# Optimization experiments

Measured on AMD Instinct MI355X. Metric: run time of the kernel, lower is better.

Reference implementation:

```python
import jax, jax.numpy as jnp
import numpy as np

B, NP1, D = 64, 1025, 256  # N+1 tokens, feature dim d (label dim makes d+1)
N_LAYER, N_HEAD = 4, 4
VAR = 0.02


def _pad_pq(allparam):
    """Build padded (d+1)x(d+1) P_full/Q_full for all layers/heads at once.
    P_full gets a 1 at [d, d]; Q_full is zero-padded."""
    L, H, _, d, _ = allparam.shape
    Pf = (jnp.zeros((L, H, d + 1, d + 1), allparam.dtype)
          .at[:, :, :d, :d].set(allparam[:, :, 0])
          .at[:, :, d, d].set(1.0))
    Qf = (jnp.zeros((L, H, d + 1, d + 1), allparam.dtype)
          .at[:, :, :d, :d].set(allparam[:, :, 1]))
    return Pf, Qf


def setup_inputs() -> dict:
    key = jax.random.key(0)
    k1, k2 = jax.random.split(key)
    Z = jax.random.normal(k1, (B, NP1, D + 1), dtype=jnp.float32)
    allparam = jax.random.normal(k2, (N_LAYER, N_HEAD, 2, D, D), dtype=jnp.float32) * VAR
    return {"Z": Z, "allparam": allparam}


def reference(Z, allparam):
    Bb, Np1, dp1 = Z.shape
    N = Np1 - 1
    Pf, Qf = _pad_pq(allparam)  # (L, H, d+1, d+1)
    # mask A = diag(1,...,1,0): equivalent to zeroing the last key token
    mask = jnp.ones((Np1,), Z.dtype).at[N].set(0.0)
    for l in range(allparam.shape[0]):
        # attn[b,h,n,m] = Z[b,n,:] @ Q_full[h] @ Z[b,m,:]
        attn = jnp.einsum('bni,hij,bmj->bhnm', Z, Qf[l], Z)
        attn = jax.nn.relu(attn)
        # key[b,h,m,i] = P_full[h] @ Z[b,m,:], last token masked out (A matrix)
        key_t = jnp.einsum('hij,bmj->bhmi', Pf[l], Z) * mask[None, None, :, None]
        # sum over heads fused into the einsum reduction; scale by 1/N
        res = jnp.einsum('bhnm,bhmi->bni', attn, key_t) / N
        Z = Z + res  # residual connection
    return Z
```

## Files before the change

### kernel.cpp

```cpp
#include <hip/hip_runtime.h>
#include <cstdint>
#include <cstddef>

#define B_    64
#define NP1   1025
#define N_    1024
#define D_    256
#define DP1   257
#define L_    4
#define H_    4
#define MT    1024
#define NCHE  32
#define IPAD  272
#define TR_   1024

typedef __bf16 bf16;
typedef bf16 bf16x4 __attribute__((ext_vector_type(4)));
typedef bf16 bf16x8 __attribute__((ext_vector_type(8)));
typedef float f32x4 __attribute__((ext_vector_type(4)));

__device__ __forceinline__ f32x4 mfma16(bf16x8 a, bf16x8 b, f32x4 c) {
    return __builtin_amdgcn_mfma_f32_16x16x32_bf16(a, b, c, 0, 0, 0);
}

__device__ __forceinline__ void async16(const void* g, void* l) {
    __builtin_amdgcn_global_load_lds(
        (const __attribute__((address_space(1))) void*)g,
        (__attribute__((address_space(3))) void*)l, 16, 0, 0);
}

__global__ void k_prep_pq(const float* __restrict__ ap,
                          bf16* __restrict__ Pb, bf16* __restrict__ Qt) {
    int idx = blockIdx.x * 256 + threadIdx.x;
    int j  = idx & 255;
    int i  = (idx >> 8) & 255;
    int lh = idx >> 16;
    const float* base = ap + (size_t)lh * 2 * D_ * D_;
    float p = base[i * D_ + j];
    float q = base[D_ * D_ + i * D_ + j];
    Pb[((size_t)lh * D_ + i) * D_ + j] = (bf16)p;
    Qt[((size_t)lh * D_ + j) * D_ + i] = (bf16)q;
}

__global__ __launch_bounds__(256) void k_zbt(const float* __restrict__ Z,
                                             bf16* __restrict__ Zb,
                                             bf16* __restrict__ ZbT) {
    __shared__ float t[64][65];
    int m0 = blockIdx.x * 64, j0 = blockIdx.y * 64, b = blockIdx.z;
    int c = threadIdx.x & 63, r0 = threadIdx.x >> 6;
#pragma unroll
    for (int s = 0; s < 16; s++) {
        int r = s * 4 + r0;
        int j = j0 + c;
        float v = (j < DP1) ? Z[((size_t)b * NP1 + m0 + r) * DP1 + j] : 0.f;
        t[r][c] = v;
        if (j < D_) Zb[((size_t)b * N_ + m0 + r) * D_ + j] = (bf16)v;
    }
    __syncthreads();
#pragma unroll
    for (int s = 0; s < 16; s++) {
        int rr = s * 4 + r0;
        int j = j0 + rr;
        if (j < DP1)
            ZbT[((size_t)b * DP1 + j) * MT + m0 + c] = (bf16)t[c][rr];
    }
}

__global__ __launch_bounds__(512, 1) void k_attn(const bf16* __restrict__ Zb,
                                                 const bf16* __restrict__ ZbT,
                                                 const bf16* __restrict__ Qt,
                                                 bf16* __restrict__ T,
                                                 bf16* __restrict__ Tlab,
                                                 int layer) {
    __shared__ bf16 zbS[2][32][256];
    __shared__ bf16 ztS[2][IPAD][32];
    __shared__ bf16 sl[8][32][40];

    const int tid  = threadIdx.x;
    const int id   = blockIdx.x;
    const int wave = tid >> 6, lane = tid & 63;
    const int quad = lane >> 4, l16 = lane & 15;

    const int xcd = id & 7, u = id >> 3;
    const int b   = xcd + 8 * (u & 7);
    const int bx  = u >> 3;
    const int n0w = bx * 256 + wave * 32;

    const bf16* Zbb  = Zb  + (size_t)b * N_ * D_;
    const bf16* ZbTb = ZbT + (size_t)b * DP1 * MT;

    const int zrow  = wave * 2 + (lane >> 5);
    const int zscol = ((lane & 31) ^ (zrow & 7)) * 8;
    const int krow  = wave * 16 + (lane >> 2);
    const int kscol = ((lane & 3) ^ ((lane >> 3) & 3)) * 8;
    const int xs    = l16 & 7;
    const int kf    = (l16 >> 1) & 3;

    auto stage = [&](int mc_, int p_) {
        int m0 = mc_ * 32;
        const bf16* zsrc = Zbb + (size_t)(m0 + zrow) * D_ + zscol;
#pragma unroll
        for (int t = 0; t < 2; t++)
            async16(zsrc + (size_t)t * 16 * D_, &zbS[p_][t * 16 + wave * 2][0]);
        const bf16* ksrc = ZbTb + (size_t)krow * MT + m0 + kscol;
#pragma unroll
        for (int t = 0; t < 2; t++)
            async16(ksrc + (size_t)t * 128 * MT, &ztS[p_][t * 128 + wave * 16][0]);
        if (wave == 0)
            async16(ksrc + (size_t)256 * MT, &ztS[p_][256][0]);
    };

    int p = 0;

    for (int h = 0; h < H_; h++) {
        const bf16* Qth = Qt + (size_t)(layer * H_ + h) * D_ * D_;

        if (h == 0) stage(0, 0);

        f32x4 acc[2][17];
#pragma unroll
        for (int ns = 0; ns < 2; ns++)
#pragma unroll
            for (int it = 0; it < 17; it++) acc[ns][it] = (f32x4){0.f, 0.f, 0.f, 0.f};

        bf16x8 zqa[2][8];
#pragma unroll 2
        for (int jc = 0; jc < 8; jc++) {
            f32x4 c00 = (f32x4){0.f,0.f,0.f,0.f}, c01 = c00, c10 = c00, c11 = c00;
#pragma unroll
            for (int kc = 0; kc < 8; kc++) {
                const bf16* qb = Qth + (size_t)(jc * 32 + l16) * D_ + kc * 32 + quad * 8;
                const bf16* az = Zbb + (size_t)(n0w + l16) * D_ + kc * 32 + quad * 8;
                bf16x8 q0 = *(const bf16x8*)(qb);
                bf16x8 q1 = *(const bf16x8*)(qb + 16 * D_);
                bf16x8 a0 = *(const bf16x8*)(az);
                bf16x8 a1 = *(const bf16x8*)(az + 16 * D_);
                c00 = mfma16(q0, a0, c00);
                c01 = mfma16(q0, a1, c01);
                c10 = mfma16(q1, a0, c10);
                c11 = mfma16(q1, a1, c11);
            }
            f32x4 cv[2][2] = {{c00, c01}, {c10, c11}};
#pragma unroll
            for (int jt = 0; jt < 2; jt++)
#pragma unroll
                for (int ns = 0; ns < 2; ns++) {
                    bf16x4 pk;
#pragma unroll
                    for (int r = 0; r < 4; r++) pk[r] = (bf16)cv[jt][ns][r];
                    *(bf16x4*)(&sl[wave][ns * 16 + l16][jt * 16 + quad * 4]) = pk;
                }
#pragma unroll
            for (int ns = 0; ns < 2; ns++)
                zqa[ns][jc] = *(const bf16x8*)(&sl[wave][ns * 16 + l16][quad * 8]);
        }

        if (h == 0) {
            asm volatile("s_waitcnt vmcnt(0)" ::: "memory");
            __builtin_amdgcn_s_barrier();
            __builtin_amdgcn_sched_barrier(0);
        }

        for (int cc = 0; cc < NCHE; cc++) {
            const bool haveNext = (cc + 1 < NCHE);
            if (haveNext) {
                int mcn = (h & 1) ? (NCHE - 2 - cc) : (cc + 1);
                stage(mcn, p ^ 1);
                if (wave == 0) asm volatile("s_waitcnt vmcnt(5)" ::: "memory");
                else           asm volatile("s_waitcnt vmcnt(4)" ::: "memory");
            } else {
                asm volatile("s_waitcnt vmcnt(0)" ::: "memory");
            }
            __builtin_amdgcn_s_barrier();
            __builtin_amdgcn_sched_barrier(0);

#pragma unroll
            for (int mt = 0; mt < 2; mt++) {
                f32x4 st0 = (f32x4){0.f,0.f,0.f,0.f}, st1 = st0;
                const bf16* zr = &zbS[p][mt * 16 + l16][0];
                __builtin_amdgcn_s_setprio(1);
#pragma unroll
                for (int kc = 0; kc < 8; kc++) {
                    bf16x8 az = *(const bf16x8*)(zr + (((kc * 4 + quad) ^ xs) * 8));
                    st0 = mfma16(az, zqa[0][kc], st0);
                    st1 = mfma16(az, zqa[1][kc], st1);
                }
                __builtin_amdgcn_s_setprio(0);
                bf16x4 p0, p1;
#pragma unroll
                for (int r = 0; r < 4; r++) {
                    p0[r] = (bf16)(st0[r] > 0.f ? st0[r] : 0.f);
                    p1[r] = (bf16)(st1[r] > 0.f ? st1[r] : 0.f);
                }
                *(bf16x4*)(&sl[wave][l16][mt * 16 + quad * 4])      = p0;
                *(bf16x4*)(&sl[wave][16 + l16][mt * 16 + quad * 4]) = p1;
            }
            bf16x8 sfrag[2];
#pragma unroll
            for (int ns = 0; ns < 2; ns++)
                sfrag[ns] = *(const bf16x8*)(&sl[wave][ns * 16 + l16][quad * 8]);

            __builtin_amdgcn_s_setprio(1);
#pragma unroll
            for (int it = 0; it < 17; it++) {
                const bf16* kr = &ztS[p][it * 16 + l16][0];
                bf16x8 bk = *(const bf16x8*)(kr + ((quad ^ kf) * 8));
                acc[0][it] = mfma16(sfrag[0], bk, acc[0][it]);
                acc[1][it] = mfma16(sfrag[1], bk, acc[1][it]);
            }
            __builtin_amdgcn_s_setprio(0);

            __builtin_amdgcn_sched_barrier(0);
            __builtin_amdgcn_s_barrier();
            if (haveNext) p ^= 1;
        }

        bf16* Th  = T    + (size_t)(b * H_ + h) * TR_ * D_;
        bf16* Tlh = Tlab + (size_t)(b * H_ + h) * TR_;
#pragma unroll
        for (int ns = 0; ns < 2; ns++)
#pragma unroll
            for (int it = 0; it < 17; it++)
#pragma unroll
                for (int r = 0; r < 4; r++) {
                    int n = n0w + ns * 16 + quad * 4 + r;
                    float v = acc[ns][it][r];
                    if (it < 16)
                        Th[(size_t)n * D_ + it * 16 + l16] = (bf16)v;
                    else if (l16 == 0)
                        Tlh[n] = (bf16)v;
                }
    }
}

__global__ __launch_bounds__(256, 2) void k_post(const bf16* __restrict__ T,
                                                 const bf16* __restrict__ Tlab,
                                                 const bf16* __restrict__ Pb,
                                                 const bf16* __restrict__ Zb,
                                                 const bf16* __restrict__ ZbT,
                                                 const bf16* __restrict__ Qt,
                                                 float* __restrict__ Z, int layer) {
    __shared__ float lz1[256];
    __shared__ float lzq[256];
    __shared__ float lsS[1024];
    __shared__ float lT[256];
    __shared__ float llab[256];

    const int tid  = threadIdx.x;
    const int id   = blockIdx.x;

    if (id >= 512) {
        const int b = id - 512;
        const bf16* Zbb  = Zb  + (size_t)b * N_ * D_;
        const bf16* tr   = ZbT + ((size_t)b * DP1 + tid) * MT;
        const bf16* zlab = ZbT + ((size_t)b * DP1 + D_) * MT;
        lz1[tid] = Z[((size_t)b * NP1 + N_) * DP1 + tid];
        float outacc = 0.f, labacc = 0.f;
        __syncthreads();
        for (int h = 0; h < H_; h++) {
            const bf16* Qth = Qt + (size_t)(layer * H_ + h) * D_ * D_;
            const bf16* Ph  = Pb + (size_t)(layer * H_ + h) * D_ * D_;
            {
                float a = 0.f;
                const bf16* qr = Qth + (size_t)tid * D_;
                for (int i8 = 0; i8 < 32; i8++) {
                    bf16x8 q = *(const bf16x8*)(qr + i8 * 8);
#pragma unroll
                    for (int k = 0; k < 8; k++) a += lz1[i8 * 8 + k] * (float)q[k];
                }
                lzq[tid] = a;
            }
            __syncthreads();
            for (int m = tid; m < N_; m += 256) {
                float a = 0.f;
                const bf16* zr = Zbb + (size_t)m * D_;
                for (int j8 = 0; j8 < 32; j8++) {
                    bf16x8 z8 = *(const bf16x8*)(zr + j8 * 8);
#pragma unroll
                    for (int k = 0; k < 8; k++) a += lzq[j8 * 8 + k] * (float)z8[k];
                }
                lsS[m] = a > 0.f ? a : 0.f;
            }
            __syncthreads();
            {
                float tv = 0.f;
                for (int m8 = 0; m8 < 128; m8++) {
                    bf16x8 t8 = *(const bf16x8*)(tr + m8 * 8);
#pragma unroll
                    for (int k = 0; k < 8; k++) tv += lsS[m8 * 8 + k] * (float)t8[k];
                }
                lT[tid] = tv;
            }
            for (int m = tid; m < N_; m += 256)
                labacc += lsS[m] * (float)zlab[m];
            __syncthreads();
            {
                const bf16* pr = Ph + (size_t)tid * D_;
                for (int j8 = 0; j8 < 32; j8++) {
                    bf16x8 p8 = *(const bf16x8*)(pr + j8 * 8);
#pragma unroll
                    for (int k = 0; k < 8; k++) outacc += lT[j8 * 8 + k] * (float)p8[k];
                }
            }
            __syncthreads();
        }
        const float inv = 1.0f / (float)N_;
        Z[((size_t)b * NP1 + N_) * DP1 + tid] += outacc * inv;
        llab[tid] = labacc;
        __syncthreads();
        if (tid == 0) {
            float s = 0.f;
            for (int t = 0; t < 256; t++) s += llab[t];
            Z[((size_t)b * NP1 + N_) * DP1 + D_] += s * inv;
        }
        return;
    }

    const int wave = tid >> 6, lane = tid & 63;
    const int quad = lane >> 4, l16 = lane & 15;
    const int xcd = id & 7, u = id >> 3;
    const int b   = xcd + 8 * (u & 3) + 32 * (u >> 5);
    const int bx  = (u >> 2) & 7;
    const int n0w = bx * 128 + wave * 32;

    f32x4 acc[2][16];
#pragma unroll
    for (int ns = 0; ns < 2; ns++)
#pragma unroll
        for (int it = 0; it < 16; it++) acc[ns][it] = (f32x4){0.f, 0.f, 0.f, 0.f};

    for (int h = 0; h < H_; h++) {
        const bf16* Th = T  + (size_t)(b * H_ + h) * TR_ * D_;
        const bf16* Ph = Pb + (size_t)(layer * H_ + h) * D_ * D_;
#pragma unroll 2
        for (int kc = 0; kc < 8; kc++) {
            bf16x8 af[2];
#pragma unroll
            for (int ns = 0; ns < 2; ns++) {
                int row = n0w + ns * 16 + l16;
                af[ns] = *(const bf16x8*)(Th + (size_t)row * D_ + kc * 32 + quad * 8);
            }
#pragma unroll
            for (int it = 0; it < 16; it++) {
                bf16x8 bp = *(const bf16x8*)(Ph + (size_t)(it * 16 + l16) * D_ + kc * 32 + quad * 8);
                acc[0][it] = mfma16(af[0], bp, acc[0][it]);
                acc[1][it] = mfma16(af[1], bp, acc[1][it]);
            }
        }
    }

    const float inv = 1.0f / (float)N_;
#pragma unroll
    for (int ns = 0; ns < 2; ns++)
#pragma unroll
        for (int it = 0; it < 16; it++)
#pragma unroll
            for (int r = 0; r < 4; r++) {
                int n = n0w + ns * 16 + quad * 4 + r;
                int i = it * 16 + l16;
                Z[((size_t)b * NP1 + n) * DP1 + i] += acc[ns][it][r] * inv;
            }
    if (tid < 128) {
        int n = bx * 128 + tid;
        float s = 0.f;
#pragma unroll
        for (int h = 0; h < H_; h++)
            s += (float)Tlab[(size_t)(b * H_ + h) * TR_ + n];
        Z[((size_t)b * NP1 + n) * DP1 + D_] += s * inv;
    }
}

extern "C" void kernel_launch(void* const* d_in, const int* in_sizes, int n_in,
                              void* d_out, int out_size, void* d_ws, size_t ws_size,
                              hipStream_t stream) {
    const float* Zin = (const float*)d_in[0];
    const float* ap  = (const float*)d_in[1];
    float* Z = (float*)d_out;

    char* ws = (char*)d_ws;
    const size_t sz_Zb  = (size_t)B_ * N_ * D_ * sizeof(bf16);
    const size_t sz_ZbT = (size_t)B_ * DP1 * MT * sizeof(bf16);
    const size_t sz_T   = (size_t)B_ * H_ * TR_ * D_ * sizeof(bf16);
    const size_t sz_Tl  = (size_t)B_ * H_ * TR_ * sizeof(bf16);
    const size_t sz_P   = (size_t)L_ * H_ * D_ * D_ * sizeof(bf16);
    bf16* Zb  = (bf16*)ws;
    bf16* ZbT = (bf16*)(ws + sz_Zb);
    bf16* Tb  = (bf16*)(ws + sz_Zb + sz_ZbT);
    bf16* Tl  = (bf16*)(ws + sz_Zb + sz_ZbT + sz_T);
    bf16* Pb  = (bf16*)(ws + sz_Zb + sz_ZbT + sz_T + sz_Tl);
    bf16* Qt  = (bf16*)(ws + sz_Zb + sz_ZbT + sz_T + sz_Tl + sz_P);

    hipMemcpyAsync(Z, Zin, (size_t)B_ * NP1 * DP1 * sizeof(float),
                   hipMemcpyDeviceToDevice, stream);

    k_prep_pq<<<dim3((L_ * H_ * D_ * D_) / 256), 256, 0, stream>>>(ap, Pb, Qt);

    for (int l = 0; l < L_; l++) {
        k_zbt<<<dim3(N_ / 64, 5, B_), 256, 0, stream>>>(Z, Zb, ZbT);
        k_attn<<<dim3(256), 512, 0, stream>>>(Zb, ZbT, Qt, Tb, Tl, l);
        k_post<<<dim3(576), 256, 0, stream>>>(Tb, Tl, Pb, Zb, ZbT, Qt, Z, l);
    }
}
```

Measured before the change: 3.679 ms.

## Fuse bf16 Z conversion into post epilogue and move last-token row into attention

The per-layer k_zbt launch is removed. k_post's epilogue now writes the updated Z directly into the bf16 row-major and transposed copies used by the next layer, so k_zbt runs only once before the loop. The last-token (query N) computation moves from k_post into 64 extra blocks of k_attn. k_post splits its output dimension in half, giving twice as many blocks with half the accumulators and an occupancy hint of 4. The aim is to avoid re-reading and re-writing the full Z tensor each layer and to improve load balance, at the cost of scattered 4-element transposed stores in the epilogue and duplicated T reads across the two output halves.

```diff
diff --git a/kernel.cpp b/kernel.cpp
--- a/kernel.cpp
+++ b/kernel.cpp
@@ -69,6 +69,8 @@
 __global__ __launch_bounds__(512, 1) void k_attn(const bf16* __restrict__ Zb,
                                                  const bf16* __restrict__ ZbT,
                                                  const bf16* __restrict__ Qt,
+                                                 const bf16* __restrict__ Pb,
+                                                 float* __restrict__ Z,
                                                  bf16* __restrict__ T,
                                                  bf16* __restrict__ Tlab,
                                                  int layer) {
@@ -80,6 +82,71 @@
     const int id   = blockIdx.x;
     const int wave = tid >> 6, lane = tid & 63;
     const int quad = lane >> 4, l16 = lane & 15;
+
+    if (id >= 256) {
+        const int bq = id - 256;
+        float* lz1 = (float*)&zbS[0][0][0];
+        float* lzq = lz1 + 256;
+        float* lsS = lzq + 256;
+        float* lT  = lsS + 1024;
+        const bf16* Zbb2  = Zb  + (size_t)bq * N_ * D_;
+        const bf16* ZbTb2 = ZbT + (size_t)bq * DP1 * MT;
+        if (tid < 256) lz1[tid] = Z[((size_t)bq * NP1 + N_) * DP1 + tid];
+        float outacc = 0.f, labacc = 0.f;
+        __syncthreads();
+        for (int h = 0; h < H_; h++) {
+            const bf16* Qth = Qt + (size_t)(layer * H_ + h) * D_ * D_;
+            const bf16* Ph  = Pb + (size_t)(layer * H_ + h) * D_ * D_;
+            if (tid < 256) {
+                float a = 0.f;
+                const bf16* qr = Qth + (size_t)tid * D_;
+                for (int i8 = 0; i8 < 32; i8++) {
+                    bf16x8 q = *(const bf16x8*)(qr + i8 * 8);
+#pragma unroll
+                    for (int k = 0; k < 8; k++) a += lz1[i8 * 8 + k] * (float)q[k];
+                }
+                lzq[tid] = a;
+            }
+            __syncthreads();
+            for (int m = tid; m < N_; m += 512) {
+                float a = 0.f;
+                const bf16* zr = Zbb2 + (size_t)m * D_;
+                for (int j8 = 0; j8 < 32; j8++) {
+                    bf16x8 z8 = *(const bf16x8*)(zr + j8 * 8);
+#pragma unroll
+                    for (int k = 0; k < 8; k++) a += lzq[j8 * 8 + k] * (float)z8[k];
+                }
+                lsS[m] = a > 0.f ? a : 0.f;
+            }
+            __syncthreads();
+            if (tid < DP1) {
+                float tv = 0.f;
+                const bf16* tr2 = ZbTb2 + (size_t)tid * MT;
+                for (int m8 = 0; m8 < 128; m8++) {
+                    bf16x8 t8 = *(const bf16x8*)(tr2 + m8 * 8);
+#pragma unroll
+                    for (int k = 0; k < 8; k++) tv += lsS[m8 * 8 + k] * (float)t8[k];
+                }
+                lT[tid] = tv;
+            }
+            __syncthreads();
+            if (tid < 256) {
+                const bf16* pr = Ph + (size_t)tid * D_;
+                for (int j8 = 0; j8 < 32; j8++) {
+                    bf16x8 p8 = *(const bf16x8*)(pr + j8 * 8);
+#pragma unroll
+                    for (int k = 0; k < 8; k++) outacc += lT[j8 * 8 + k] * (float)p8[k];
+                }
+            } else if (tid == 256) {
+                labacc += lT[256];
+            }
+            __syncthreads();
+        }
+        const float inv = 1.0f / (float)N_;
+        if (tid < 256)  Z[((size_t)bq * NP1 + N_) * DP1 + tid] += outacc * inv;
+        if (tid == 256) Z[((size_t)bq * NP1 + N_) * DP1 + D_]  += labacc * inv;
+        return;
+    }
 
     const int xcd = id & 7, u = id >> 3;
     const int b   = xcd + 8 * (u & 7);
@@ -233,101 +300,29 @@
     }
 }
 
-__global__ __launch_bounds__(256, 2) void k_post(const bf16* __restrict__ T,
+__global__ __launch_bounds__(256, 4) void k_post(const bf16* __restrict__ T,
                                                  const bf16* __restrict__ Tlab,
                                                  const bf16* __restrict__ Pb,
-                                                 const bf16* __restrict__ Zb,
-                                                 const bf16* __restrict__ ZbT,
-                                                 const bf16* __restrict__ Qt,
-                                                 float* __restrict__ Z, int layer) {
-    __shared__ float lz1[256];
-    __shared__ float lzq[256];
-    __shared__ float lsS[1024];
-    __shared__ float lT[256];
-    __shared__ float llab[256];
-
+                                                 float* __restrict__ Z,
+                                                 bf16* __restrict__ Zb,
+                                                 bf16* __restrict__ ZbT,
+                                                 int layer) {
     const int tid  = threadIdx.x;
     const int id   = blockIdx.x;
-
-    if (id >= 512) {
-        const int b = id - 512;
-        const bf16* Zbb  = Zb  + (size_t)b * N_ * D_;
-        const bf16* tr   = ZbT + ((size_t)b * DP1 + tid) * MT;
-        const bf16* zlab = ZbT + ((size_t)b * DP1 + D_) * MT;
-        lz1[tid] = Z[((size_t)b * NP1 + N_) * DP1 + tid];
-        float outacc = 0.f, labacc = 0.f;
-        __syncthreads();
-        for (int h = 0; h < H_; h++) {
-            const bf16* Qth = Qt + (size_t)(layer * H_ + h) * D_ * D_;
-            const bf16* Ph  = Pb + (size_t)(layer * H_ + h) * D_ * D_;
-            {
-                float a = 0.f;
-                const bf16* qr = Qth + (size_t)tid * D_;
-                for (int i8 = 0; i8 < 32; i8++) {
-                    bf16x8 q = *(const bf16x8*)(qr + i8 * 8);
-#pragma unroll
-                    for (int k = 0; k < 8; k++) a += lz1[i8 * 8 + k] * (float)q[k];
-                }
-                lzq[tid] = a;
-            }
-            __syncthreads();
-            for (int m = tid; m < N_; m += 256) {
-                float a = 0.f;
-                const bf16* zr = Zbb + (size_t)m * D_;
-                for (int j8 = 0; j8 < 32; j8++) {
-                    bf16x8 z8 = *(const bf16x8*)(zr + j8 * 8);
-#pragma unroll
-                    for (int k = 0; k < 8; k++) a += lzq[j8 * 8 + k] * (float)z8[k];
-                }
-                lsS[m] = a > 0.f ? a : 0.f;
-            }
-            __syncthreads();
-            {
-                float tv = 0.f;
-                for (int m8 = 0; m8 < 128; m8++) {
-                    bf16x8 t8 = *(const bf16x8*)(tr + m8 * 8);
-#pragma unroll
-                    for (int k = 0; k < 8; k++) tv += lsS[m8 * 8 + k] * (float)t8[k];
-                }
-                lT[tid] = tv;
-            }
-            for (int m = tid; m < N_; m += 256)
-                labacc += lsS[m] * (float)zlab[m];
-            __syncthreads();
-            {
-                const bf16* pr = Ph + (size_t)tid * D_;
-                for (int j8 = 0; j8 < 32; j8++) {
-                    bf16x8 p8 = *(const bf16x8*)(pr + j8 * 8);
-#pragma unroll
-                    for (int k = 0; k < 8; k++) outacc += lT[j8 * 8 + k] * (float)p8[k];
-                }
-            }
-            __syncthreads();
-        }
-        const float inv = 1.0f / (float)N_;
-        Z[((size_t)b * NP1 + N_) * DP1 + tid] += outacc * inv;
-        llab[tid] = labacc;
-        __syncthreads();
-        if (tid == 0) {
-            float s = 0.f;
-            for (int t = 0; t < 256; t++) s += llab[t];
-            Z[((size_t)b * NP1 + N_) * DP1 + D_] += s * inv;
-        }
-        return;
-    }
-
     const int wave = tid >> 6, lane = tid & 63;
     const int quad = lane >> 4, l16 = lane & 15;
     const int xcd = id & 7, u = id >> 3;
-    const int b   = xcd + 8 * (u & 3) + 32 * (u >> 5);
+    const int b   = xcd + 8 * (u & 3) + 32 * ((u >> 5) & 1);
     const int bx  = (u >> 2) & 7;
+    const int ih  = u >> 6;
     const int n0w = bx * 128 + wave * 32;
-
-    f32x4 acc[2][16];
+    const int i0  = ih * 128;
+
+    f32x4 acc[2][8];
 #pragma unroll
     for (int ns = 0; ns < 2; ns++)
 #pragma unroll
-        for (int it = 0; it < 16; it++) acc[ns][it] = (f32x4){0.f, 0.f, 0.f, 0.f};
+        for (int it = 0; it < 8; it++) acc[ns][it] = (f32x4){0.f, 0.f, 0.f, 0.f};
 
     for (int h = 0; h < H_; h++) {
         const bf16* Th = T  + (size_t)(b * H_ + h) * TR_ * D_;
@@ -341,8 +336,8 @@
                 af[ns] = *(const bf16x8*)(Th + (size_t)row * D_ + kc * 32 + quad * 8);
             }
 #pragma unroll
-            for (int it = 0; it < 16; it++) {
-                bf16x8 bp = *(const bf16x8*)(Ph + (size_t)(it * 16 + l16) * D_ + kc * 32 + quad * 8);
+            for (int it = 0; it < 8; it++) {
+                bf16x8 bp = *(const bf16x8*)(Ph + (size_t)(i0 + it * 16 + l16) * D_ + kc * 32 + quad * 8);
                 acc[0][it] = mfma16(af[0], bp, acc[0][it]);
                 acc[1][it] = mfma16(af[1], bp, acc[1][it]);
             }
@@ -350,23 +345,36 @@
     }
 
     const float inv = 1.0f / (float)N_;
+    const bool wnext = (layer < L_ - 1);
 #pragma unroll
     for (int ns = 0; ns < 2; ns++)
 #pragma unroll
-        for (int it = 0; it < 16; it++)
+        for (int it = 0; it < 8; it++) {
+            const int i = i0 + it * 16 + l16;
+            const int nbase = n0w + ns * 16 + quad * 4;
+            bf16x4 zpk;
 #pragma unroll
             for (int r = 0; r < 4; r++) {
-                int n = n0w + ns * 16 + quad * 4 + r;
-                int i = it * 16 + l16;
-                Z[((size_t)b * NP1 + n) * DP1 + i] += acc[ns][it][r] * inv;
-            }
-    if (tid < 128) {
+                int n = nbase + r;
+                size_t zi = ((size_t)b * NP1 + n) * DP1 + i;
+                float v = Z[zi] + acc[ns][it][r] * inv;
+                Z[zi] = v;
+                zpk[r] = (bf16)v;
+                if (wnext) Zb[((size_t)b * N_ + n) * D_ + i] = (bf16)v;
+            }
+            if (wnext)
+                *(bf16x4*)(&ZbT[((size_t)b * DP1 + i) * MT + nbase]) = zpk;
+        }
+    if (ih == 0 && tid < 128) {
         int n = bx * 128 + tid;
         float s = 0.f;
 #pragma unroll
         for (int h = 0; h < H_; h++)
             s += (float)Tlab[(size_t)(b * H_ + h) * TR_ + n];
-        Z[((size_t)b * NP1 + n) * DP1 + D_] += s * inv;
+        size_t zi = ((size_t)b * NP1 + n) * DP1 + D_;
+        float v = Z[zi] + s * inv;
+        Z[zi] = v;
+        if (wnext) ZbT[((size_t)b * DP1 + D_) * MT + n] = (bf16)v;
     }
 }
 
@@ -394,10 +402,10 @@
                    hipMemcpyDeviceToDevice, stream);
 
     k_prep_pq<<<dim3((L_ * H_ * D_ * D_) / 256), 256, 0, stream>>>(ap, Pb, Qt);
+    k_zbt<<<dim3(N_ / 64, 5, B_), 256, 0, stream>>>(Z, Zb, ZbT);
 
     for (int l = 0; l < L_; l++) {
-        k_zbt<<<dim3(N_ / 64, 5, B_), 256, 0, stream>>>(Z, Zb, ZbT);
-        k_attn<<<dim3(256), 512, 0, stream>>>(Zb, ZbT, Qt, Tb, Tl, l);
-        k_post<<<dim3(576), 256, 0, stream>>>(Tb, Tl, Pb, Zb, ZbT, Qt, Z, l);
-    }
-}
+        k_attn<<<dim3(320), 512, 0, stream>>>(Zb, ZbT, Qt, Pb, Z, Tb, Tl, l);
+        k_post<<<dim3(1024), 256, 0, stream>>>(Tb, Tl, Pb, Z, Zb, ZbT, l);
+    }
+}
```

After: 3.590 ms. 1.02x faster.
